# Performance work log

Measured on AMD Instinct MI355X. Metric: run time of the kernel, lower is better.

## Reference

```python
import jax, jax.numpy as jnp
import numpy as np

N_NODES = 100000
N_EDGES = 3200000
N_GRAPHS = 1000
HID = 64
L = 4  # num_unit


def setup_inputs() -> dict:
    key = jax.random.key(0)
    ks = jax.random.split(key, 16)
    x = jax.random.normal(ks[0], (N_NODES, 4), dtype=jnp.float32)
    edge_index = jax.random.randint(ks[1], (2, N_EDGES), 0, N_NODES, dtype=jnp.int64)
    edge_attr = jax.random.uniform(ks[2], (N_EDGES,), dtype=jnp.float32)
    batch = jnp.sort(jax.random.randint(ks[3], (N_NODES,), 0, N_GRAPHS, dtype=jnp.int64))
    s = 1.0 / np.sqrt(HID)
    inp = {
        'x': x, 'edge_index': edge_index, 'edge_attr': edge_attr, 'batch': batch,
        'emb_w': jax.random.normal(ks[4], (4, HID), jnp.float32) * 0.5,
        'emb_b': jnp.zeros((HID,), jnp.float32),
        'conv_w1': jax.random.normal(ks[5], (L, HID, HID), jnp.float32) * s,
        'conv_b1': jnp.zeros((L, HID), jnp.float32),
        'conv_w2': jax.random.normal(ks[6], (L, HID, HID), jnp.float32) * s,
        'conv_w3': jax.random.normal(ks[7], (L, HID, HID), jnp.float32) * s,
        'conv_b3': jnp.zeros((L, HID), jnp.float32),
        'lin1_w': jax.random.normal(ks[8], (HID, HID), jnp.float32) * s,
        'lin1_b': jnp.zeros((HID,), jnp.float32),
        'lin2_w': jax.random.normal(ks[9], (HID, 3), jnp.float32) * s,
        'lin2_b': jnp.zeros((3,), jnp.float32),
    }
    return inp


def _forward(x, edge_index, edge_attr, batch,
             emb_w, emb_b, conv_w1, conv_b1, conv_w2, conv_w3, conv_b3,
             lin1_w, lin1_b, lin2_w, lin2_b):
    src, dst = edge_index[0], edge_index[1]
    ew = edge_attr[:, None]  # [E,1]
    h = x @ emb_w + emb_b  # node_emb; dropout omitted (eval mode)
    for l in range(conv_w1.shape[0]):
        # LEConv: out_i = sum_{j->i} w_ji * (lin1(x_j) - lin2(x_i)) + lin3(x_i)
        a = h @ conv_w1[l] + conv_b1[l]
        b = h @ conv_w2[l]  # no bias
        msg = (a[src] - b[dst]) * ew  # [E, HID]
        agg = jax.ops.segment_sum(msg, dst, num_segments=h.shape[0])
        h = jax.nn.relu(agg + h @ conv_w3[l] + conv_b3[l])
    # global mean pool over graphs
    sums = jax.ops.segment_sum(h, batch, num_segments=N_GRAPHS)
    cnt = jax.ops.segment_sum(jnp.ones((h.shape[0],), h.dtype), batch, num_segments=N_GRAPHS)
    graph_x = sums / jnp.maximum(cnt, 1.0)[:, None]
    pred = jax.nn.relu(graph_x @ lin1_w + lin1_b) @ lin2_w + lin2_b
    return pred


def reference(x, edge_index, edge_attr, batch, emb_w, emb_b,
              conv_w1, conv_b1, conv_w2, conv_w3, conv_b3,
              lin1_w, lin1_b, lin2_w, lin2_b):
    return _forward(x, edge_index, edge_attr, batch, emb_w, emb_b,
                    conv_w1, conv_b1, conv_w2, conv_w3, conv_b3,
                    lin1_w, lin1_b, lin2_w, lin2_b)
```

## Files before the change

kernel.cpp:

```cpp
#include <hip/hip_runtime.h>

#define N_NODES 100000
#define N_EDGES 3200000
#define N_GRAPHS 1000
#define NLAYER 4
#define NB 391
#define G1 782
#define EPB 4096
#define PCAP 16384

typedef __attribute__((ext_vector_type(8))) short bf16x8;
typedef __attribute__((ext_vector_type(4))) float f32x4;

static __device__ __forceinline__ unsigned f2bf(float f) {
  unsigned u = __float_as_uint(f);
  return (u + 0x7fffu + ((u >> 16) & 1u)) >> 16;
}
static __device__ __forceinline__ float bf2f_lo(unsigned u) {
  return __uint_as_float(u << 16);
}
static __device__ __forceinline__ float bf2f_hi(unsigned u) {
  return __uint_as_float(u & 0xffff0000u);
}

__global__ __launch_bounds__(256) void embed_kernel(
    const float* __restrict__ x, const float* __restrict__ emb_w,
    const float* __restrict__ emb_b, unsigned short* __restrict__ h_bf)
{
  int t = blockIdx.x * 256 + threadIdx.x;
  if (t >= N_NODES * 64) return;
  int c = t & 63, v = t >> 6;
  float4 xv = ((const float4*)x)[v];
  float acc = emb_b[c];
  acc = fmaf(xv.x, emb_w[0 * 64 + c], acc);
  acc = fmaf(xv.y, emb_w[1 * 64 + c], acc);
  acc = fmaf(xv.z, emb_w[2 * 64 + c], acc);
  acc = fmaf(xv.w, emb_w[3 * 64 + c], acc);
  h_bf[t] = (unsigned short)f2bf(acc);
}

__global__ __launch_bounds__(256) void bhist_kernel(
    const int* __restrict__ ei, int* __restrict__ bhist)
{
  __shared__ unsigned hist[NB];
  for (int i = threadIdx.x; i < NB; i += 256) hist[i] = 0;
  __syncthreads();
  int base = blockIdx.x * EPB;
#pragma unroll
  for (int i = 0; i < 16; ++i) {
    int e = base + i * 256 + threadIdx.x;
    if (e < N_EDGES) atomicAdd(&hist[((unsigned)ei[N_EDGES + e]) >> 8], 1u);
  }
  __syncthreads();
  for (int i = threadIdx.x; i < NB; i += 256)
    bhist[blockIdx.x * NB + i] = (int)hist[i];
}

__global__ __launch_bounds__(256) void colscan_kernel(
    int* __restrict__ bhist, int* __restrict__ tots)
{
  int b = blockIdx.x;
  __shared__ int s[256];
  __shared__ int carry;
  if (threadIdx.x == 0) carry = 0;
  __syncthreads();
  for (int c0 = 0; c0 < G1; c0 += 256) {
    int g = c0 + threadIdx.x;
    int v = (g < G1) ? bhist[g * NB + b] : 0;
    s[threadIdx.x] = v;
    __syncthreads();
    for (int off = 1; off < 256; off <<= 1) {
      int y = (threadIdx.x >= off) ? s[threadIdx.x - off] : 0;
      __syncthreads();
      s[threadIdx.x] += y;
      __syncthreads();
    }
    if (g < G1) bhist[g * NB + b] = carry + s[threadIdx.x] - v;
    __syncthreads();
    if (threadIdx.x == 0) carry += s[255];
    __syncthreads();
  }
  if (threadIdx.x == 0) tots[b] = carry;
}

__global__ __launch_bounds__(512) void bucketscan_kernel(
    const int* __restrict__ tots, int* __restrict__ bb)
{
  __shared__ int s[512];
  int x = ((int)threadIdx.x < NB) ? tots[threadIdx.x] : 0;
  s[threadIdx.x] = x;
  __syncthreads();
  for (int off = 1; off < 512; off <<= 1) {
    int y = (threadIdx.x >= off) ? s[threadIdx.x - off] : 0;
    __syncthreads();
    s[threadIdx.x] += y;
    __syncthreads();
  }
  if ((int)threadIdx.x < NB) bb[threadIdx.x] = s[threadIdx.x] - x;
  if (threadIdx.x == 0) bb[NB] = N_EDGES;
}

__global__ __launch_bounds__(256) void bscatter_kernel(
    const int* __restrict__ ei, const float* __restrict__ ea,
    const int* __restrict__ bhist, const int* __restrict__ bb,
    int2* __restrict__ tmp)
{
  __shared__ unsigned hist[NB];
  __shared__ int lbase[NB];
  __shared__ unsigned cur[NB];
  __shared__ int2 stage[EPB];
  __shared__ unsigned short bid[EPB];
  __shared__ int carry;
  __shared__ int sbuf[256];
  int tid = threadIdx.x;
  int base = blockIdx.x * EPB;

  for (int i = tid; i < NB; i += 256) hist[i] = 0;
  if (tid == 0) carry = 0;
  __syncthreads();

#pragma unroll
  for (int i = 0; i < 16; ++i) {
    int e = base + i * 256 + tid;
    if (e < N_EDGES) atomicAdd(&hist[((unsigned)ei[N_EDGES + e]) >> 8], 1u);
  }
  __syncthreads();

  for (int c0 = 0; c0 < NB; c0 += 256) {
    int g = c0 + tid;
    int v = (g < NB) ? (int)hist[g] : 0;
    sbuf[tid] = v;
    __syncthreads();
    for (int off = 1; off < 256; off <<= 1) {
      int y = (tid >= off) ? sbuf[tid - off] : 0;
      __syncthreads();
      sbuf[tid] += y;
      __syncthreads();
    }
    if (g < NB) {
      int ex = carry + sbuf[tid] - v;
      lbase[g] = ex;
      cur[g] = (unsigned)ex;
    }
    __syncthreads();
    if (tid == 0) carry += sbuf[255];
    __syncthreads();
  }

#pragma unroll
  for (int i = 0; i < 16; ++i) {
    int e = base + i * 256 + tid;
    if (e < N_EDGES) {
      int d = ei[N_EDGES + e];
      unsigned bkt = ((unsigned)d) >> 8;
      unsigned lp = atomicAdd(&cur[bkt], 1u);
      stage[lp] = make_int2(ei[e] | ((d & 255) << 17), __float_as_int(ea[e]));
      bid[lp] = (unsigned short)bkt;
    }
  }
  __syncthreads();

  int nE = min(EPB, N_EDGES - base);
  for (int i = tid; i < nE; i += 256) {
    int bkt = (int)bid[i];
    int gpos = bb[bkt] + bhist[blockIdx.x * NB + bkt] + (i - lbase[bkt]);
    tmp[gpos] = stage[i];
  }
}

__global__ __launch_bounds__(256) void bucket_sort_kernel(
    const int* __restrict__ bb, const int2* __restrict__ tmp,
    unsigned* __restrict__ csr, int* __restrict__ row_off, float* __restrict__ degw)
{
  int j = blockIdx.x;
  int b0 = bb[j], b1 = bb[j + 1];
  int nE = b1 - b0;
  __shared__ unsigned hist[256];
  __shared__ float dws[256];
  __shared__ int scanbuf[256];
  __shared__ unsigned cur[256];
  __shared__ unsigned short perm[PCAP];
  int t = threadIdx.x;
  hist[t] = 0;
  dws[t] = 0.f;
  __syncthreads();
  for (int i = t; i < nE; i += 256) {
    int2 r = tmp[b0 + i];
    int bin = ((unsigned)r.x) >> 17;
    atomicAdd(&hist[bin], 1u);
    atomicAdd(&dws[bin], __int_as_float(r.y));
  }
  __syncthreads();
  int v = (int)hist[t];
  scanbuf[t] = v;
  __syncthreads();
  for (int off = 1; off < 256; off <<= 1) {
    int y = (t >= off) ? scanbuf[t - off] : 0;
    __syncthreads();
    scanbuf[t] += y;
    __syncthreads();
  }
  int myexcl = scanbuf[t] - v;
  cur[t] = (unsigned)myexcl;
  int vnode = (j << 8) + t;
  if (vnode < N_NODES) {
    row_off[vnode] = b0 + myexcl;
    degw[vnode] = dws[t];
  }
  if (j == NB - 1 && t == 0) row_off[N_NODES] = N_EDGES;
  __syncthreads();

  if (nE <= PCAP) {
    for (int i = t; i < nE; i += 256) {
      int2 r = tmp[b0 + i];
      int bin = ((unsigned)r.x) >> 17;
      unsigned p = atomicAdd(&cur[bin], 1u);
      perm[p] = (unsigned short)i;
    }
    __syncthreads();
    for (int q = t; q < nE; q += 256) {
      int2 r = tmp[b0 + (int)perm[q]];
      unsigned q15 = (unsigned)(__int_as_float(r.y) * 32768.0f);
      csr[b0 + q] = ((unsigned)r.x & 0x1FFFFu) | (q15 << 17);
    }
  } else {
    for (int i = t; i < nE; i += 256) {
      int2 r = tmp[b0 + i];
      int bin = ((unsigned)r.x) >> 17;
      unsigned p = atomicAdd(&cur[bin], 1u);
      unsigned q15 = (unsigned)(__int_as_float(r.y) * 32768.0f);
      csr[b0 + (int)p] = ((unsigned)r.x & 0x1FFFFu) | (q15 << 17);
    }
  }
}

__global__ __launch_bounds__(256) void wswz_kernel(
    const float* __restrict__ cw1, const float* __restrict__ cw2,
    const float* __restrict__ cw3, unsigned* __restrict__ wswz)
{
  int l = blockIdx.x;
  const float* w1 = cw1 + l * 4096;
  const float* w2 = cw2 + l * 4096;
  const float* w3 = cw3 + l * 4096;
  unsigned* outp = wswz + l * 6144;
  int tid = threadIdx.x;
  int n = tid & 63;
  int gofs = tid >> 6;
  for (int it = 0; it < 24; ++it) {
    int g = it * 4 + gofs;
    int m = g >> 5;
    int kp = g & 31;
    int k = kp * 2;
    const float* W = (m == 0) ? w2 : (m == 1) ? w3 : w1;
    unsigned lo = f2bf(W[k * 64 + n]);
    unsigned hi = f2bf(W[(k + 1) * 64 + n]);
    int c = k >> 5;
    int kk = k & 31;
    int lane = ((kk >> 3) << 4) | (n & 15);
    int j2 = (kk & 7) >> 1;
    int t = n >> 4;
    outp[(((m * 2 + c) * 4 + t) << 8) | (lane << 2) | j2] = lo | (hi << 16);
  }
}

__global__ __launch_bounds__(256) void matvec3_mfma_kernel(
    const unsigned short* __restrict__ h_bf,
    const unsigned* __restrict__ wz,
    const float* __restrict__ b1, const float* __restrict__ b3,
    const float* __restrict__ degw,
    unsigned short* __restrict__ a_bf, unsigned short* __restrict__ cc_bf)
{
  int gw = (blockIdx.x * 256 + threadIdx.x) >> 6;
  int lane = threadIdx.x & 63;
  int quad = lane >> 4;
  int col = lane & 15;
  int nb = gw * 16;
  if (nb >= N_NODES) return;

  int arow = nb + col;
  if (arow >= N_NODES) arow = N_NODES - 1;
  const bf16x8* ap = (const bf16x8*)(h_bf + (size_t)arow * 64 + quad * 8);
  bf16x8 af0 = ap[0];
  bf16x8 af1 = ap[4];

  float dwr[4];
#pragma unroll
  for (int r = 0; r < 4; ++r) {
    int row = nb + quad * 4 + r;
    dwr[r] = degw[row < N_NODES ? row : 0];
  }

#pragma unroll
  for (int t = 0; t < 4; ++t) {
    const bf16x8* b20 = (const bf16x8*)&wz[((0 * 4 + t) << 8) + lane * 4];
    const bf16x8* b21 = (const bf16x8*)&wz[((1 * 4 + t) << 8) + lane * 4];
    const bf16x8* b30 = (const bf16x8*)&wz[((2 * 4 + t) << 8) + lane * 4];
    const bf16x8* b31 = (const bf16x8*)&wz[((3 * 4 + t) << 8) + lane * 4];
    const bf16x8* b10 = (const bf16x8*)&wz[((4 * 4 + t) << 8) + lane * 4];
    const bf16x8* b11 = (const bf16x8*)&wz[((5 * 4 + t) << 8) + lane * 4];

    f32x4 z = {0.f, 0.f, 0.f, 0.f};
    f32x4 acc2 = __builtin_amdgcn_mfma_f32_16x16x32_bf16(af0, *b20, z, 0, 0, 0);
    acc2 = __builtin_amdgcn_mfma_f32_16x16x32_bf16(af1, *b21, acc2, 0, 0, 0);
    f32x4 cc;
#pragma unroll
    for (int r = 0; r < 4; ++r) cc[r] = -dwr[r] * acc2[r];
    cc = __builtin_amdgcn_mfma_f32_16x16x32_bf16(af0, *b30, cc, 0, 0, 0);
    cc = __builtin_amdgcn_mfma_f32_16x16x32_bf16(af1, *b31, cc, 0, 0, 0);
    float bb3 = b3[t * 16 + col];
#pragma unroll
    for (int r = 0; r < 4; ++r) {
      int row = nb + quad * 4 + r;
      if (row < N_NODES)
        cc_bf[(size_t)row * 64 + t * 16 + col] = (unsigned short)f2bf(cc[r] + bb3);
    }

    float bb1 = b1[t * 16 + col];
    f32x4 a1 = {bb1, bb1, bb1, bb1};
    a1 = __builtin_amdgcn_mfma_f32_16x16x32_bf16(af0, *b10, a1, 0, 0, 0);
    a1 = __builtin_amdgcn_mfma_f32_16x16x32_bf16(af1, *b11, a1, 0, 0, 0);
#pragma unroll
    for (int r = 0; r < 4; ++r) {
      int row = nb + quad * 4 + r;
      if (row < N_NODES)
        a_bf[(size_t)row * 64 + t * 16 + col] = (unsigned short)f2bf(a1[r]);
    }
  }
}

__global__ __launch_bounds__(256) void agg_kernel(
    const uint2* __restrict__ a2, const uint2* __restrict__ cc2,
    const int* __restrict__ row_off, const unsigned* __restrict__ csr,
    float4* __restrict__ h4, unsigned short* __restrict__ h_bf, int write_h)
{
  int wave = (blockIdx.x * 256 + threadIdx.x) >> 6;
  int lane = threadIdx.x & 63;
  int sg = lane >> 4;
  int li = lane & 15;
  int v = wave * 4 + sg;
  bool valid = v < N_NODES;
  int vc = valid ? v : N_NODES - 1;
  int base = row_off[vc];
  int ecnt = valid ? (row_off[vc + 1] - base) : 0;
  int emax = ecnt;
  emax = max(emax, __shfl_xor(emax, 16));
  emax = max(emax, __shfl_xor(emax, 32));

  float4 acc = make_float4(0.f, 0.f, 0.f, 0.f);
  if (valid) {
    uint2 cu = cc2[(size_t)vc * 16 + li];
    acc.x = bf2f_lo(cu.x);
    acc.y = bf2f_hi(cu.x);
    acc.z = bf2f_lo(cu.y);
    acc.w = bf2f_hi(cu.y);
  }

  int full = emax & ~15;
  int c0 = 0;
  for (; c0 < full; c0 += 16) {
    int idx = c0 + li;
    unsigned er = (idx < ecnt) ? csr[base + idx] : 0u;
#pragma unroll
    for (int j = 0; j < 16; ++j) {
      unsigned r = (unsigned)__shfl((int)er, sg * 16 + j);
      int s = (int)(r & 0x1FFFFu);
      float w = (float)(r >> 17) * (1.0f / 32768.0f);
      uint2 u = a2[(size_t)s * 16 + li];
      acc.x = fmaf(w, bf2f_lo(u.x), acc.x);
      acc.y = fmaf(w, bf2f_hi(u.x), acc.y);
      acc.z = fmaf(w, bf2f_lo(u.y), acc.z);
      acc.w = fmaf(w, bf2f_hi(u.y), acc.w);
    }
  }
  int rem = emax - full;
  if (rem > 0) {
    int idx = c0 + li;
    unsigned er = (idx < ecnt) ? csr[base + idx] : 0u;
    for (int j = 0; j < rem; ++j) {
      unsigned r = (unsigned)__shfl((int)er, sg * 16 + j);
      int s = (int)(r & 0x1FFFFu);
      float w = (float)(r >> 17) * (1.0f / 32768.0f);
      uint2 u = a2[(size_t)s * 16 + li];
      acc.x = fmaf(w, bf2f_lo(u.x), acc.x);
      acc.y = fmaf(w, bf2f_hi(u.x), acc.y);
      acc.z = fmaf(w, bf2f_lo(u.y), acc.z);
      acc.w = fmaf(w, bf2f_hi(u.y), acc.w);
    }
  }
  if (valid) {
    acc.x = fmaxf(acc.x, 0.f);
    acc.y = fmaxf(acc.y, 0.f);
    acc.z = fmaxf(acc.z, 0.f);
    acc.w = fmaxf(acc.w, 0.f);
    if (write_h) h4[(size_t)v * 16 + li] = acc;
    uint2 p;
    p.x = f2bf(acc.x) | (f2bf(acc.y) << 16);
    p.y = f2bf(acc.z) | (f2bf(acc.w) << 16);
    ((uint2*)h_bf)[(size_t)v * 16 + li] = p;
  }
}

__global__ __launch_bounds__(256) void head_kernel(
    const float* __restrict__ h, const int* __restrict__ batch,
    const float* __restrict__ l1w, const float* __restrict__ l1b,
    const float* __restrict__ l2w, const float* __restrict__ l2b,
    float* __restrict__ out)
{
  int g = (blockIdx.x * 256 + threadIdx.x) >> 6;
  int lane = threadIdx.x & 63;
  if (g >= N_GRAPHS) return;
  int lo = 0, hi = N_NODES;
  while (lo < hi) { int mid = (lo + hi) >> 1; if (batch[mid] < g) lo = mid + 1; else hi = mid; }
  int start = lo;
  hi = N_NODES;
  while (lo < hi) { int mid = (lo + hi) >> 1; if (batch[mid] < g + 1) lo = mid + 1; else hi = mid; }
  int end = lo;

  float sum = 0.f;
  for (int v = start; v < end; ++v) sum += h[(size_t)v * 64 + lane];
  float cntf = (float)(end - start);
  float gx = sum / fmaxf(cntf, 1.f);

  float acc = l1b[lane];
  for (int k = 0; k < 64; ++k) {
    float gxk = __shfl(gx, k);
    acc = fmaf(gxk, l1w[k * 64 + lane], acc);
  }
  float t = fmaxf(acc, 0.f);
  float p0 = t * l2w[lane * 3 + 0];
  float p1 = t * l2w[lane * 3 + 1];
  float p2 = t * l2w[lane * 3 + 2];
  for (int off = 32; off > 0; off >>= 1) {
    p0 += __shfl_down(p0, off);
    p1 += __shfl_down(p1, off);
    p2 += __shfl_down(p2, off);
  }
  if (lane == 0) {
    out[g * 3 + 0] = p0 + l2b[0];
    out[g * 3 + 1] = p1 + l2b[1];
    out[g * 3 + 2] = p2 + l2b[2];
  }
}

extern "C" void kernel_launch(void* const* d_in, const int* in_sizes, int n_in,
                              void* d_out, int out_size, void* d_ws, size_t ws_size,
                              hipStream_t stream)
{
  (void)in_sizes; (void)n_in; (void)out_size; (void)ws_size;
  const float* x     = (const float*)d_in[0];
  const int*   ei    = (const int*)d_in[1];
  const float* ea    = (const float*)d_in[2];
  const int*   batch = (const int*)d_in[3];
  const float* emb_w = (const float*)d_in[4];
  const float* emb_b = (const float*)d_in[5];
  const float* cw1   = (const float*)d_in[6];
  const float* cb1   = (const float*)d_in[7];
  const float* cw2   = (const float*)d_in[8];
  const float* cw3   = (const float*)d_in[9];
  const float* cb3   = (const float*)d_in[10];
  const float* l1w   = (const float*)d_in[11];
  const float* l1b   = (const float*)d_in[12];
  const float* l2w   = (const float*)d_in[13];
  const float* l2b   = (const float*)d_in[14];
  float* out = (float*)d_out;

  char* wsb = (char*)d_ws;
  size_t off = 0;
  auto alloc = [&](size_t bytes) {
    char* p = wsb + off;
    off = (off + bytes + 255) & ~(size_t)255;
    return p;
  };
  float* h       = (float*)alloc(sizeof(float) * (size_t)N_NODES * 64);
  unsigned short* h_bf = (unsigned short*)alloc(sizeof(short) * (size_t)N_NODES * 64);
  unsigned short* a_bf = (unsigned short*)alloc(sizeof(short) * (size_t)N_NODES * 64);
  unsigned short* cc_bf = (unsigned short*)alloc(sizeof(short) * (size_t)N_NODES * 64);
  unsigned* csr  = (unsigned*)alloc(sizeof(unsigned) * (size_t)N_EDGES);
  int*   row_off = (int*)alloc(sizeof(int) * (N_NODES + 1));
  float* degw    = (float*)alloc(sizeof(float) * N_NODES);
  int*   bhist   = (int*)alloc(sizeof(int) * (size_t)G1 * NB);
  int*   tots    = (int*)alloc(sizeof(int) * NB);
  int*   bb      = (int*)alloc(sizeof(int) * (NB + 1));
  unsigned* wswz = (unsigned*)alloc(sizeof(unsigned) * NLAYER * 6144);
  int2* tmp = (int2*)h;

  embed_kernel<<<(N_NODES * 64 + 255) / 256, 256, 0, stream>>>(x, emb_w, emb_b, h_bf);
  wswz_kernel<<<NLAYER, 256, 0, stream>>>(cw1, cw2, cw3, wswz);
  bhist_kernel<<<G1, 256, 0, stream>>>(ei, bhist);
  colscan_kernel<<<NB, 256, 0, stream>>>(bhist, tots);
  bucketscan_kernel<<<1, 512, 0, stream>>>(tots, bb);
  bscatter_kernel<<<G1, 256, 0, stream>>>(ei, ea, bhist, bb, tmp);
  bucket_sort_kernel<<<NB, 256, 0, stream>>>(bb, tmp, csr, row_off, degw);

  int agg_blocks = (N_NODES + 15) / 16;
  int mv_blocks = (N_NODES / 16 + 3) / 4 + 1;
  for (int l = 0; l < NLAYER; ++l) {
    matvec3_mfma_kernel<<<mv_blocks, 256, 0, stream>>>(
        h_bf, wswz + l * 6144, cb1 + l * 64, cb3 + l * 64, degw, a_bf, cc_bf);
    agg_kernel<<<agg_blocks, 256, 0, stream>>>(
        (const uint2*)a_bf, (const uint2*)cc_bf, row_off, csr, (float4*)h,
        h_bf, (l == NLAYER - 1) ? 1 : 0);
  }

  head_kernel<<<(N_GRAPHS * 64 + 255) / 256, 256, 0, stream>>>(
      h, batch, l1w, l1b, l2w, l2b, out);
}
```

Baseline: 533.3 us.

## Sort nodes by degree for aggregation and simplify CSR build with atomic bucket cursors

The CSR build drops the per-block histogram matrix and column scans. It uses global atomic bucket totals and per-block atomic cursor reservation, with smaller buckets of 128 nodes and 2048 edges per block. A new degree counting-sort pass builds a node permutation so each wave aggregates nodes of equal degree. This removes divergence on the padded max-degree loop, and the shuffle becomes ds_bpermute. In exchange it adds several small kernels and scattered node access in the aggregation.

```diff
diff --git a/kernel.cpp b/kernel.cpp
--- a/kernel.cpp
+++ b/kernel.cpp
@@ -4,10 +4,12 @@
 #define N_EDGES 3200000
 #define N_GRAPHS 1000
 #define NLAYER 4
-#define NB 391
-#define G1 782
-#define EPB 4096
-#define PCAP 16384
+#define NB 782
+#define BBITS 7
+#define EPB2 2048
+#define G1 1563
+#define GH 782
+#define PCAP 6144
 
 typedef __attribute__((ext_vector_type(8))) short bf16x8;
 typedef __attribute__((ext_vector_type(4))) float f32x4;
@@ -21,6 +23,12 @@
 }
 static __device__ __forceinline__ float bf2f_hi(unsigned u) {
   return __uint_as_float(u & 0xffff0000u);
+}
+
+__global__ __launch_bounds__(256) void zero_kernel(int* __restrict__ p, int n)
+{
+  int i = blockIdx.x * 256 + threadIdx.x;
+  if (i < n) p[i] = 0;
 }
 
 __global__ __launch_bounds__(256) void embed_kernel(
@@ -39,90 +47,74 @@
   h_bf[t] = (unsigned short)f2bf(acc);
 }
 
-__global__ __launch_bounds__(256) void bhist_kernel(
-    const int* __restrict__ ei, int* __restrict__ bhist)
+__global__ __launch_bounds__(256) void hist1_kernel(
+    const int* __restrict__ ei, int* __restrict__ tots)
 {
   __shared__ unsigned hist[NB];
   for (int i = threadIdx.x; i < NB; i += 256) hist[i] = 0;
   __syncthreads();
-  int base = blockIdx.x * EPB;
+  int base = blockIdx.x * 4096;
 #pragma unroll
   for (int i = 0; i < 16; ++i) {
     int e = base + i * 256 + threadIdx.x;
-    if (e < N_EDGES) atomicAdd(&hist[((unsigned)ei[N_EDGES + e]) >> 8], 1u);
-  }
-  __syncthreads();
-  for (int i = threadIdx.x; i < NB; i += 256)
-    bhist[blockIdx.x * NB + i] = (int)hist[i];
-}
-
-__global__ __launch_bounds__(256) void colscan_kernel(
-    int* __restrict__ bhist, int* __restrict__ tots)
-{
-  int b = blockIdx.x;
-  __shared__ int s[256];
+    if (e < N_EDGES) atomicAdd(&hist[((unsigned)ei[N_EDGES + e]) >> BBITS], 1u);
+  }
+  __syncthreads();
+  for (int i = threadIdx.x; i < NB; i += 256) {
+    unsigned c = hist[i];
+    if (c) atomicAdd(&tots[i], (int)c);
+  }
+}
+
+__global__ __launch_bounds__(1024) void scan1_kernel(
+    const int* __restrict__ tots, int* __restrict__ bb, int* __restrict__ gcur)
+{
+  __shared__ int s[1024];
+  int t = threadIdx.x;
+  int x = (t < NB) ? tots[t] : 0;
+  s[t] = x;
+  __syncthreads();
+  for (int off = 1; off < 1024; off <<= 1) {
+    int y = (t >= off) ? s[t - off] : 0;
+    __syncthreads();
+    s[t] += y;
+    __syncthreads();
+  }
+  if (t < NB) {
+    int ex = s[t] - x;
+    bb[t] = ex;
+    gcur[t] = ex;
+  }
+  if (t == 0) bb[NB] = N_EDGES;
+}
+
+__global__ __launch_bounds__(256) void bscatter2_kernel(
+    const int* __restrict__ ei, const float* __restrict__ ea,
+    int* __restrict__ gcur, int2* __restrict__ tmp)
+{
+  __shared__ unsigned hist[NB];
+  __shared__ int dif[NB];
+  __shared__ int2 stage[EPB2];
+  __shared__ unsigned short bid[EPB2];
+  __shared__ int sbuf[256];
   __shared__ int carry;
-  if (threadIdx.x == 0) carry = 0;
-  __syncthreads();
-  for (int c0 = 0; c0 < G1; c0 += 256) {
-    int g = c0 + threadIdx.x;
-    int v = (g < G1) ? bhist[g * NB + b] : 0;
-    s[threadIdx.x] = v;
-    __syncthreads();
-    for (int off = 1; off < 256; off <<= 1) {
-      int y = (threadIdx.x >= off) ? s[threadIdx.x - off] : 0;
-      __syncthreads();
-      s[threadIdx.x] += y;
-      __syncthreads();
-    }
-    if (g < G1) bhist[g * NB + b] = carry + s[threadIdx.x] - v;
-    __syncthreads();
-    if (threadIdx.x == 0) carry += s[255];
-    __syncthreads();
-  }
-  if (threadIdx.x == 0) tots[b] = carry;
-}
-
-__global__ __launch_bounds__(512) void bucketscan_kernel(
-    const int* __restrict__ tots, int* __restrict__ bb)
-{
-  __shared__ int s[512];
-  int x = ((int)threadIdx.x < NB) ? tots[threadIdx.x] : 0;
-  s[threadIdx.x] = x;
-  __syncthreads();
-  for (int off = 1; off < 512; off <<= 1) {
-    int y = (threadIdx.x >= off) ? s[threadIdx.x - off] : 0;
-    __syncthreads();
-    s[threadIdx.x] += y;
-    __syncthreads();
-  }
-  if ((int)threadIdx.x < NB) bb[threadIdx.x] = s[threadIdx.x] - x;
-  if (threadIdx.x == 0) bb[NB] = N_EDGES;
-}
-
-__global__ __launch_bounds__(256) void bscatter_kernel(
-    const int* __restrict__ ei, const float* __restrict__ ea,
-    const int* __restrict__ bhist, const int* __restrict__ bb,
-    int2* __restrict__ tmp)
-{
-  __shared__ unsigned hist[NB];
-  __shared__ int lbase[NB];
-  __shared__ unsigned cur[NB];
-  __shared__ int2 stage[EPB];
-  __shared__ unsigned short bid[EPB];
-  __shared__ int carry;
-  __shared__ int sbuf[256];
   int tid = threadIdx.x;
-  int base = blockIdx.x * EPB;
+  int base = blockIdx.x * EPB2;
 
   for (int i = tid; i < NB; i += 256) hist[i] = 0;
   if (tid == 0) carry = 0;
   __syncthreads();
 
 #pragma unroll
-  for (int i = 0; i < 16; ++i) {
+  for (int i = 0; i < 8; ++i) {
     int e = base + i * 256 + tid;
-    if (e < N_EDGES) atomicAdd(&hist[((unsigned)ei[N_EDGES + e]) >> 8], 1u);
+    if (e < N_EDGES) atomicAdd(&hist[((unsigned)ei[N_EDGES + e]) >> BBITS], 1u);
+  }
+  __syncthreads();
+
+  for (int b = tid; b < NB; b += 256) {
+    int c = (int)hist[b];
+    dif[b] = c ? atomicAdd(&gcur[b], c) : 0;
   }
   __syncthreads();
 
@@ -139,8 +131,8 @@
     }
     if (g < NB) {
       int ex = carry + sbuf[tid] - v;
-      lbase[g] = ex;
-      cur[g] = (unsigned)ex;
+      hist[g] = (unsigned)ex;
+      dif[g] -= ex;
     }
     __syncthreads();
     if (tid == 0) carry += sbuf[255];
@@ -148,41 +140,39 @@
   }
 
 #pragma unroll
-  for (int i = 0; i < 16; ++i) {
+  for (int i = 0; i < 8; ++i) {
     int e = base + i * 256 + tid;
     if (e < N_EDGES) {
       int d = ei[N_EDGES + e];
-      unsigned bkt = ((unsigned)d) >> 8;
-      unsigned lp = atomicAdd(&cur[bkt], 1u);
-      stage[lp] = make_int2(ei[e] | ((d & 255) << 17), __float_as_int(ea[e]));
+      unsigned bkt = ((unsigned)d) >> BBITS;
+      unsigned lp = atomicAdd(&hist[bkt], 1u);
+      stage[lp] = make_int2(ei[e] | ((d & 127) << 17), __float_as_int(ea[e]));
       bid[lp] = (unsigned short)bkt;
     }
   }
   __syncthreads();
 
-  int nE = min(EPB, N_EDGES - base);
+  int nE = min(EPB2, N_EDGES - base);
   for (int i = tid; i < nE; i += 256) {
     int bkt = (int)bid[i];
-    int gpos = bb[bkt] + bhist[blockIdx.x * NB + bkt] + (i - lbase[bkt]);
-    tmp[gpos] = stage[i];
-  }
-}
-
-__global__ __launch_bounds__(256) void bucket_sort_kernel(
+    tmp[dif[bkt] + i] = stage[i];
+  }
+}
+
+__global__ __launch_bounds__(256) void bucket_sort2_kernel(
     const int* __restrict__ bb, const int2* __restrict__ tmp,
     unsigned* __restrict__ csr, int* __restrict__ row_off, float* __restrict__ degw)
 {
   int j = blockIdx.x;
   int b0 = bb[j], b1 = bb[j + 1];
   int nE = b1 - b0;
-  __shared__ unsigned hist[256];
-  __shared__ float dws[256];
+  __shared__ unsigned hist[128];
+  __shared__ float dws[128];
   __shared__ int scanbuf[256];
-  __shared__ unsigned cur[256];
+  __shared__ unsigned cur[128];
   __shared__ unsigned short perm[PCAP];
   int t = threadIdx.x;
-  hist[t] = 0;
-  dws[t] = 0.f;
+  if (t < 128) { hist[t] = 0; dws[t] = 0.f; }
   __syncthreads();
   for (int i = t; i < nE; i += 256) {
     int2 r = tmp[b0 + i];
@@ -191,7 +181,7 @@
     atomicAdd(&dws[bin], __int_as_float(r.y));
   }
   __syncthreads();
-  int v = (int)hist[t];
+  int v = (t < 128) ? (int)hist[t] : 0;
   scanbuf[t] = v;
   __syncthreads();
   for (int off = 1; off < 256; off <<= 1) {
@@ -201,11 +191,13 @@
     __syncthreads();
   }
   int myexcl = scanbuf[t] - v;
-  cur[t] = (unsigned)myexcl;
-  int vnode = (j << 8) + t;
-  if (vnode < N_NODES) {
-    row_off[vnode] = b0 + myexcl;
-    degw[vnode] = dws[t];
+  if (t < 128) {
+    cur[t] = (unsigned)myexcl;
+    int vnode = (j << BBITS) + t;
+    if (vnode < N_NODES) {
+      row_off[vnode] = b0 + myexcl;
+      degw[vnode] = dws[t];
+    }
   }
   if (j == NB - 1 && t == 0) row_off[N_NODES] = N_EDGES;
   __syncthreads();
@@ -230,6 +222,79 @@
       unsigned p = atomicAdd(&cur[bin], 1u);
       unsigned q15 = (unsigned)(__int_as_float(r.y) * 32768.0f);
       csr[b0 + (int)p] = ((unsigned)r.x & 0x1FFFFu) | (q15 << 17);
+    }
+  }
+}
+
+__global__ __launch_bounds__(256) void dhist_kernel(
+    const int* __restrict__ row_off, int* __restrict__ dhist)
+{
+  __shared__ unsigned h[256];
+  int t = threadIdx.x;
+  h[t] = 0;
+  __syncthreads();
+  int v0 = (blockIdx.x * 256 + t) * 4;
+#pragma unroll
+  for (int k = 0; k < 4; ++k) {
+    int v = v0 + k;
+    if (v < N_NODES) {
+      int d = row_off[v + 1] - row_off[v];
+      atomicAdd(&h[min(d, 255)], 1u);
+    }
+  }
+  __syncthreads();
+  unsigned c = h[t];
+  if (c) atomicAdd(&dhist[t], (int)c);
+}
+
+__global__ __launch_bounds__(256) void dscan_kernel(
+    const int* __restrict__ dhist, int* __restrict__ dcur)
+{
+  __shared__ int s[256];
+  int t = threadIdx.x;
+  int v = dhist[t];
+  s[t] = v;
+  __syncthreads();
+  for (int off = 1; off < 256; off <<= 1) {
+    int y = (t >= off) ? s[t - off] : 0;
+    __syncthreads();
+    s[t] += y;
+    __syncthreads();
+  }
+  dcur[t] = s[t] - v;
+}
+
+__global__ __launch_bounds__(256) void dperm_kernel(
+    const int* __restrict__ row_off, int* __restrict__ dcur,
+    int* __restrict__ nodeperm)
+{
+  __shared__ unsigned h[256];
+  __shared__ unsigned lcur[256];
+  int t = threadIdx.x;
+  h[t] = 0;
+  __syncthreads();
+  int v0 = (blockIdx.x * 256 + t) * 4;
+  int dloc[4];
+#pragma unroll
+  for (int k = 0; k < 4; ++k) {
+    int v = v0 + k;
+    dloc[k] = -1;
+    if (v < N_NODES) {
+      int d = min(row_off[v + 1] - row_off[v], 255);
+      dloc[k] = d;
+      atomicAdd(&h[d], 1u);
+    }
+  }
+  __syncthreads();
+  unsigned c = h[t];
+  unsigned gb = c ? (unsigned)atomicAdd(&dcur[t], (int)c) : 0u;
+  lcur[t] = gb;
+  __syncthreads();
+#pragma unroll
+  for (int k = 0; k < 4; ++k) {
+    if (dloc[k] >= 0) {
+      unsigned p = atomicAdd(&lcur[dloc[k]], 1u);
+      nodeperm[p] = v0 + k;
     }
   }
 }
@@ -331,56 +396,55 @@
 __global__ __launch_bounds__(256) void agg_kernel(
     const uint2* __restrict__ a2, const uint2* __restrict__ cc2,
     const int* __restrict__ row_off, const unsigned* __restrict__ csr,
+    const int* __restrict__ nodeperm,
     float4* __restrict__ h4, unsigned short* __restrict__ h_bf, int write_h)
 {
   int wave = (blockIdx.x * 256 + threadIdx.x) >> 6;
   int lane = threadIdx.x & 63;
   int sg = lane >> 4;
   int li = lane & 15;
-  int v = wave * 4 + sg;
-  bool valid = v < N_NODES;
-  int vc = valid ? v : N_NODES - 1;
-  int base = row_off[vc];
-  int ecnt = valid ? (row_off[vc + 1] - base) : 0;
-  int emax = ecnt;
-  emax = max(emax, __shfl_xor(emax, 16));
-  emax = max(emax, __shfl_xor(emax, 32));
+  int lsel = (lane & 48) << 2;
+  int vslot = wave * 4 + sg;
+  bool valid = vslot < N_NODES;
+  int v = nodeperm[valid ? vslot : N_NODES - 1];
+  int base = row_off[v];
+  int ecnt = valid ? (row_off[v + 1] - base) : 0;
 
   float4 acc = make_float4(0.f, 0.f, 0.f, 0.f);
   if (valid) {
-    uint2 cu = cc2[(size_t)vc * 16 + li];
+    uint2 cu = cc2[(size_t)v * 16 + li];
     acc.x = bf2f_lo(cu.x);
     acc.y = bf2f_hi(cu.x);
     acc.z = bf2f_lo(cu.y);
     acc.w = bf2f_hi(cu.y);
   }
-
-  int full = emax & ~15;
+  const uint2* ap = a2 + li;
+
+  int full = ecnt & ~15;
   int c0 = 0;
   for (; c0 < full; c0 += 16) {
-    int idx = c0 + li;
-    unsigned er = (idx < ecnt) ? csr[base + idx] : 0u;
+    int er = (int)csr[base + c0 + li];
 #pragma unroll
     for (int j = 0; j < 16; ++j) {
-      unsigned r = (unsigned)__shfl((int)er, sg * 16 + j);
+      unsigned r = (unsigned)__builtin_amdgcn_ds_bpermute(lsel | (j << 2), er);
       int s = (int)(r & 0x1FFFFu);
       float w = (float)(r >> 17) * (1.0f / 32768.0f);
-      uint2 u = a2[(size_t)s * 16 + li];
+      uint2 u = ap[(size_t)s * 16];
       acc.x = fmaf(w, bf2f_lo(u.x), acc.x);
       acc.y = fmaf(w, bf2f_hi(u.x), acc.y);
       acc.z = fmaf(w, bf2f_lo(u.y), acc.z);
       acc.w = fmaf(w, bf2f_hi(u.y), acc.w);
     }
   }
-  int rem = emax - full;
+  int rem = ecnt - full;
   if (rem > 0) {
     int idx = c0 + li;
-    unsigned er = (idx < ecnt) ? csr[base + idx] : 0u;
+    int er = (idx < ecnt) ? (int)csr[base + idx] : 0;
     for (int j = 0; j < rem; ++j) {
-      unsigned r = (unsigned)__shfl((int)er, sg * 16 + j);
+      unsigned r = (unsigned)__builtin_amdgcn_ds_bpermute(lsel | (j << 2), er);
       int s = (int)(r & 0x1FFFFu);
       float w = (float)(r >> 17) * (1.0f / 32768.0f);
-      uint2 u = a2[(size_t)s * 16 + li];
+      uint2 u = ap[(size_t)s * 16];
       acc.x = fmaf(w, bf2f_lo(u.x), acc.x);
       acc.y = fmaf(w, bf2f_hi(u.x), acc.y);
       acc.z = fmaf(w, bf2f_lo(u.y), acc.z);
@@ -478,19 +542,27 @@
   unsigned* csr  = (unsigned*)alloc(sizeof(unsigned) * (size_t)N_EDGES);
   int*   row_off = (int*)alloc(sizeof(int) * (N_NODES + 1));
   float* degw    = (float*)alloc(sizeof(float) * N_NODES);
-  int*   bhist   = (int*)alloc(sizeof(int) * (size_t)G1 * NB);
+  int*   nodeperm= (int*)alloc(sizeof(int) * N_NODES);
   int*   tots    = (int*)alloc(sizeof(int) * NB);
+  int*   dhist_g = (int*)alloc(sizeof(int) * 256);
   int*   bb      = (int*)alloc(sizeof(int) * (NB + 1));
+  int*   gcur    = (int*)alloc(sizeof(int) * NB);
+  int*   dcur    = (int*)alloc(sizeof(int) * 256);
   unsigned* wswz = (unsigned*)alloc(sizeof(unsigned) * NLAYER * 6144);
   int2* tmp = (int2*)h;
 
+  zero_kernel<<<(NB + 255) / 256, 256, 0, stream>>>(tots, NB);
+  zero_kernel<<<1, 256, 0, stream>>>(dhist_g, 256);
+
   embed_kernel<<<(N_NODES * 64 + 255) / 256, 256, 0, stream>>>(x, emb_w, emb_b, h_bf);
   wswz_kernel<<<NLAYER, 256, 0, stream>>>(cw1, cw2, cw3, wswz);
-  bhist_kernel<<<G1, 256, 0, stream>>>(ei, bhist);
-  colscan_kernel<<<NB, 256, 0, stream>>>(bhist, tots);
-  bucketscan_kernel<<<1, 512, 0, stream>>>(tots, bb);
-  bscatter_kernel<<<G1, 256, 0, stream>>>(ei, ea, bhist, bb, tmp);
-  bucket_sort_kernel<<<NB, 256, 0, stream>>>(bb, tmp, csr, row_off, degw);
+  hist1_kernel<<<GH, 256, 0, stream>>>(ei, tots);
+  scan1_kernel<<<1, 1024, 0, stream>>>(tots, bb, gcur);
+  bscatter2_kernel<<<G1, 256, 0, stream>>>(ei, ea, gcur, tmp);
+  bucket_sort2_kernel<<<NB, 256, 0, stream>>>(bb, tmp, csr, row_off, degw);
+  dhist_kernel<<<98, 256, 0, stream>>>(row_off, dhist_g);
+  dscan_kernel<<<1, 256, 0, stream>>>(dhist_g, dcur);
+  dperm_kernel<<<98, 256, 0, stream>>>(row_off, dcur, nodeperm);
 
   int agg_blocks = (N_NODES + 15) / 16;
   int mv_blocks = (N_NODES / 16 + 3) / 4 + 1;
@@ -498,7 +570,7 @@
     matvec3_mfma_kernel<<<mv_blocks, 256, 0, stream>>>(
         h_bf, wswz + l * 6144, cb1 + l * 64, cb3 + l * 64, degw, a_bf, cc_bf);
     agg_kernel<<<agg_blocks, 256, 0, stream>>>(
-        (const uint2*)a_bf, (const uint2*)cc_bf, row_off, csr, (float4*)h,
+        (const uint2*)a_bf, (const uint2*)cc_bf, row_off, csr, nodeperm, (float4*)h,
         h_bf, (l == NLAYER - 1) ? 1 : 0);
   }
 
```

New measurement: 591.5 us. +10.9%, slower.
